# Optimization experiments

Measured on AMD Instinct MI355X. Metric: run time of the kernel, lower is better.

The kernel has to match this reference:

```python
import jax, jax.numpy as jnp
import numpy as np

B, K, D, E, V, T = 128, 49, 512, 256, 10000, 20


def setup_inputs() -> dict:
    key = jax.random.key(0)
    ks = jax.random.split(key, 20)
    rn = lambda k, shape, s=0.02: jax.random.normal(k, shape, jnp.float32) * s
    lengths = jnp.sort(jax.random.randint(ks[3], (B,), 1, T + 1))[::-1]
    lengths = lengths.at[0].set(T)  # max(lengths) == T, sorted descending
    return {
        "spatial": jax.random.normal(ks[0], (B, K, D), jnp.float32),
        "global_feats": jax.random.normal(ks[1], (B, D), jnp.float32),
        "captions": jax.random.randint(ks[2], (B, T), 0, V),
        "lengths": lengths,
        "emb": rn(ks[4], (V, E), 0.05),
        "W_init_h": rn(ks[5], (D, D)), "b_init_h": jnp.zeros((D,), jnp.float32),
        "W_init_m": rn(ks[6], (D, D)), "b_init_m": jnp.zeros((D,), jnp.float32),
        "W_ih": rn(ks[7], (4 * D, E + D)), "b_ih": jnp.zeros((4 * D,), jnp.float32),
        "W_hh": rn(ks[8], (4 * D, D)), "b_hh": jnp.zeros((4 * D,), jnp.float32),
        "Wv": rn(ks[9], (K, D)), "bv": jnp.zeros((K,), jnp.float32),
        "Wg": rn(ks[10], (K, D)), "bg": jnp.zeros((K,), jnp.float32),
        "wh": rn(ks[11], (1, K)), "bh_att": jnp.zeros((1,), jnp.float32),
        "Wp": rn(ks[12], (V, D)), "bp": jnp.zeros((V,), jnp.float32),
    }


def reference(spatial, global_feats, captions, lengths, emb,
              W_init_h, b_init_h, W_init_m, b_init_m,
              W_ih, b_ih, W_hh, b_hh,
              Wv, bv, Wg, bg, wh, bh_att, Wp, bp):
    # initialize_state
    h0 = global_feats @ W_init_h.T + b_init_h  # [B,D]
    m0 = global_feats @ W_init_m.T + b_init_m
    emb_seq = emb[captions]                     # [B,T,E]
    V_proj = spatial @ Wv.T + bv                # [B,K,K] (attn hidden = k), loop-invariant

    def step(carry, xs):
        h, m = carry
        w, t = xs                               # w: [B,E]
        active = (lengths > t)[:, None]         # masked equivalent of shrinking batch
        x = jnp.concatenate([w, global_feats], axis=1)  # [B,E+D]
        gates = x @ W_ih.T + b_ih + h @ W_hh.T + b_hh   # [B,4D]
        i, f, g, o = jnp.split(gates, 4, axis=1)        # torch LSTMCell gate order
        i, f, o = jax.nn.sigmoid(i), jax.nn.sigmoid(f), jax.nn.sigmoid(o)
        g = jnp.tanh(g)
        m_new = f * m + i * g
        h_new = o * jnp.tanh(m_new)
        h = jnp.where(active, h_new, h)
        m = jnp.where(active, m_new, m)
        # spatial attention: z = w_h^T tanh(W_v V + W_g h)
        z = jnp.tanh(V_proj + (h @ Wg.T + bg)[:, None, :]) @ wh[0] + bh_att[0]  # [B,K]
        alpha = jax.nn.softmax(z, axis=1)
        c = jnp.einsum('bk,bkd->bd', alpha, spatial)
        logit = (c + h) @ Wp.T + bp             # [B,V]
        logit = jnp.where(active, logit, 0.0)
        return (h, m), logit

    xs = (emb_seq.transpose(1, 0, 2), jnp.arange(T))
    (_, _), logits = jax.lax.scan(step, (h0, m0), xs)
    return logits.transpose(1, 0, 2)            # [B,T,V]
```

## Files before the change

kernel.cpp:

```cpp
#include <hip/hip_runtime.h>
#include <hip/hip_bf16.h>
#include <math.h>

typedef __bf16 bf16;
typedef __bf16 v8bf __attribute__((ext_vector_type(8)));
typedef __bf16 v4bfv __attribute__((ext_vector_type(4)));
typedef float  v4f  __attribute__((ext_vector_type(4)));

#define B_   128
#define KK_  49
#define D_   512
#define E_   256
#define V_   10000
#define T_   20
#define NG_  2048
#define XK_  768
#define VPAD 10112
#define NP_  128
#define NBLK 64
#define LGRID 256

#define FLG_CNT    1024
#define FLG_READY  1040
#define FLG_LEADER 1056
#define FLG_DONE   1057

#define GLOAD_LDS16(gp, lp) \
    __builtin_amdgcn_global_load_lds((const __attribute__((address_space(1))) void*)(gp), \
                                     (__attribute__((address_space(3))) void*)(lp), 16, 0, 0)

__device__ inline v4bfv cvt4(float4 v) {
    v4bfv o; o[0] = (bf16)v.x; o[1] = (bf16)v.y; o[2] = (bf16)v.z; o[3] = (bf16)v.w;
    return o;
}

__device__ inline float fsig(float x) {
    return __fdividef(1.f, 1.f + __expf(-x));
}
__device__ inline float ftanh(float x) {
    return 1.f - 2.f * __fdividef(1.f, 1.f + __expf(2.f * x));
}

__global__ void prep_kernel(
    const float* __restrict__ spatial, const float* __restrict__ gfeat,
    const int* __restrict__ caps, const float* __restrict__ emb,
    const float* __restrict__ W_init_h, const float* __restrict__ b_init_h,
    const float* __restrict__ W_init_m, const float* __restrict__ b_init_m,
    const float* __restrict__ W_ih, const float* __restrict__ b_ih,
    const float* __restrict__ W_hh, const float* __restrict__ b_hh,
    const float* __restrict__ Wv, const float* __restrict__ bv,
    const float* __restrict__ Wg, const float* __restrict__ bg,
    const float* __restrict__ Wp,
    bf16* __restrict__ Wp_b, bf16* __restrict__ Whh_b, bf16* __restrict__ Wih_b,
    bf16* __restrict__ Xin_b, bf16* __restrict__ Sp_b,
    bf16* __restrict__ Wv_b, bf16* __restrict__ Wg_b,
    bf16* __restrict__ Winit2_b, bf16* __restrict__ Gf_b,
    float* __restrict__ bias_comb, float* __restrict__ bias_init,
    float* __restrict__ bv_pad, float* __restrict__ bg_pad,
    int* __restrict__ flags)
{
    const int stride = gridDim.x * blockDim.x;
    const int tid0 = blockIdx.x * blockDim.x + threadIdx.x;
    const float4 z4 = make_float4(0.f, 0.f, 0.f, 0.f);

    for (int i = tid0; i < NBLK * 32; i += stride) flags[i] = 0;

    for (int i4 = tid0; i4 < VPAD * D_ / 4; i4 += stride) {
        int row = i4 >> 7;
        float4 v = (row < V_) ? ((const float4*)Wp)[i4] : z4;
        ((v4bfv*)Wp_b)[i4] = cvt4(v);
    }
    for (int i4 = tid0; i4 < NG_ * D_ / 4; i4 += stride)
        ((v4bfv*)Whh_b)[i4] = cvt4(((const float4*)W_hh)[i4]);
    for (int i4 = tid0; i4 < NG_ * XK_ / 4; i4 += stride)
        ((v4bfv*)Wih_b)[i4] = cvt4(((const float4*)W_ih)[i4]);
    for (int i4 = tid0; i4 < T_ * B_ * XK_ / 4; i4 += stride) {
        int r = i4 / (XK_ / 4), c4 = i4 - r * (XK_ / 4);
        int c = c4 * 4;
        int t = r >> 7, b = r & 127;
        float4 v;
        if (c < E_) v = *(const float4*)&emb[(long)caps[b * T_ + t] * E_ + c];
        else        v = *(const float4*)&gfeat[(long)b * D_ + (c - E_)];
        ((v4bfv*)Xin_b)[i4] = cvt4(v);
    }
    for (int i4 = tid0; i4 < B_ * KK_ * D_ / 4; i4 += stride)
        ((v4bfv*)Sp_b)[i4] = cvt4(((const float4*)spatial)[i4]);
    for (int i4 = tid0; i4 < NP_ * D_ / 4; i4 += stride) {
        int row = i4 >> 7;
        ((v4bfv*)Wv_b)[i4] = cvt4((row < KK_) ? ((const float4*)Wv)[i4] : z4);
        ((v4bfv*)Wg_b)[i4] = cvt4((row < KK_) ? ((const float4*)Wg)[i4] : z4);
    }
    for (int i4 = tid0; i4 < 2 * D_ * D_ / 4; i4 += stride) {
        int row = i4 >> 7;
        float4 v = (row < D_) ? ((const float4*)W_init_h)[i4]
                              : ((const float4*)W_init_m)[i4 - D_ * (D_ / 4)];
        ((v4bfv*)Winit2_b)[i4] = cvt4(v);
    }
    for (int i4 = tid0; i4 < B_ * D_ / 4; i4 += stride)
        ((v4bfv*)Gf_b)[i4] = cvt4(((const float4*)gfeat)[i4]);
    for (int i = tid0; i < NG_; i += stride) bias_comb[i] = b_ih[i] + b_hh[i];
    for (int i = tid0; i < 2 * D_; i += stride)
        bias_init[i] = (i < D_) ? b_init_h[i] : b_init_m[i - D_];
    for (int i = tid0; i < NP_; i += stride) {
        bv_pad[i] = (i < KK_) ? bv[i] : 0.f;
        bg_pad[i] = (i < KK_) ? bg[i] : 0.f;
    }
}

template <int OUTMODE>
__global__ __launch_bounds__(256, 4) void gemm_bt(
    const bf16* __restrict__ A, const bf16* __restrict__ Bm,
    const float* __restrict__ bias, void* __restrict__ Cout, void* __restrict__ Cout2,
    int M, int N, int K, int out_stride, int n_real, const int* __restrict__ lengths)
{
    __shared__ bf16 As[2 * 128 * 32];
    __shared__ bf16 Bs[2 * 128 * 32];
    const int m0 = blockIdx.x * 128, n0 = blockIdx.y * 128;
    const int tid = threadIdx.x;
    const int w = tid >> 6, l = tid & 63;
    const int wm = (w >> 1) * 64, wn = (w & 1) * 64;
    const int lr = l & 15, lq = l >> 4;

    v4f acc[4][4] = {};

    for (int k0 = 0; k0 < K; k0 += 64) {
        __syncthreads();
        #pragma unroll
        for (int c = 0; c < 4; c++) {
            int u = c * 256 + tid;
            int h = u >> 9, v = u & 511;
            int row = v >> 2, kc = (v & 3) * 8;
            int u0 = c * 256 + (tid & ~63);
            GLOAD_LDS16(&A[(long)(m0 + row) * K + k0 + h * 32 + kc], &As[u0 * 8]);
            GLOAD_LDS16(&Bm[(long)(n0 + row) * K + k0 + h * 32 + kc], &Bs[u0 * 8]);
        }
        __syncthreads();
        #pragma unroll
        for (int h = 0; h < 2; h++) {
            v8bf af[4], bfv[4];
            #pragma unroll
            for (int s = 0; s < 4; s++) {
                af[s]  = *(const v8bf*)&As[h * 4096 + (wm + s * 16 + lr) * 32 + lq * 8];
                bfv[s] = *(const v8bf*)&Bs[h * 4096 + (wn + s * 16 + lr) * 32 + lq * 8];
            }
            #pragma unroll
            for (int i = 0; i < 4; i++)
                #pragma unroll
                for (int j = 0; j < 4; j++)
                    acc[i][j] = __builtin_amdgcn_mfma_f32_16x16x32_bf16(af[i], bfv[j], acc[i][j], 0, 0, 0);
        }
    }

    #pragma unroll
    for (int i = 0; i < 4; i++)
        #pragma unroll
        for (int j = 0; j < 4; j++)
            #pragma unroll
            for (int r = 0; r < 4; r++) {
                int m = m0 + wm + i * 16 + lq * 4 + r;
                int n = n0 + wn + j * 16 + lr;
                float v = acc[i][j][r];
                if (OUTMODE == 2) {
                    if (n < n_real) {
                        int t = m % T_, b = m / T_;
                        float o = (t < lengths[b]) ? (v + bias[n]) : 0.f;
                        ((float*)Cout)[(long)m * out_stride + n] = o;
                    }
                } else if (OUTMODE == 3) {
                    if (n < D_) ((bf16*)Cout)[(long)m * D_ + n] = (bf16)(v + bias[n]);
                    else ((float*)Cout2)[(long)m * D_ + n - D_] = v + bias[n];
                } else {
                    ((float*)Cout)[(long)m * out_stride + n] = v + bias[n];
                }
            }
}

__global__ __launch_bounds__(256) void lstm_persist(
    bf16* __restrict__ Hb16, const bf16* __restrict__ Whh_b,
    const float* __restrict__ Xpre, const float* __restrict__ mbuf,
    const int* __restrict__ lengths, int* __restrict__ flags)
{
    __shared__ bf16 Bl[128][520];
    __shared__ int s_info[2];
    const int tid = threadIdx.x;

    if (tid == 0) {
        int xcd;
        asm volatile("s_getreg_b32 %0, hwreg(HW_REG_XCC_ID)" : "=s"(xcd));
        xcd &= 15;
        int slot = __hip_atomic_fetch_add(&flags[FLG_CNT + xcd], 1,
                                          __ATOMIC_RELAXED, __HIP_MEMORY_SCOPE_AGENT);
        if (slot == 31) {
            int exp = 0;
            bool win = __hip_atomic_compare_exchange_strong(
                &flags[FLG_LEADER], &exp, xcd + 1,
                __ATOMIC_RELAXED, __ATOMIC_RELAXED, __HIP_MEMORY_SCOPE_AGENT);
            __hip_atomic_store(&flags[FLG_READY + xcd], win ? 1 : 2,
                               __ATOMIC_RELAXED, __HIP_MEMORY_SCOPE_AGENT);
        }
        int st;
        if (slot < 32) {
            int dn;
            do {
                st = __hip_atomic_load(&flags[FLG_READY + xcd],
                                       __ATOMIC_RELAXED, __HIP_MEMORY_SCOPE_AGENT);
                dn = __hip_atomic_load(&flags[FLG_DONE],
                                       __ATOMIC_RELAXED, __HIP_MEMORY_SCOPE_AGENT);
            } while (st == 0 && dn == 0);
            if (st == 0) st = 2;
        } else st = 2;
        s_info[0] = st;
        s_info[1] = slot;
    }
    __syncthreads();
    if (s_info[0] != 1) return;

    const int slot = s_info[1];
    const int w = tid >> 6, l = tid & 63;
    const int lr = l & 15, lq = l >> 4;
    const int rh = slot & 1;
    const int d0v = (slot >> 1) * 32;
    const int b0 = rh * 64;
    int* const prog = &flags[rh ? 64 : 0];

    for (int u = tid; u < 128 * 64; u += 256) {
        int row = u >> 6, kc = (u & 63) * 8;
        int g = row >> 5, dd = row & 31;
        *(v8bf*)&Bl[row][kc] = *(const v8bf*)&Whh_b[(long)(g * D_ + d0v + dd) * D_ + kc];
    }

    const int brow = b0 + w * 16 + lq * 4;
    float m_st[4][2], h_st[4][2], xpf[4][2][4];
    int lenr[4];
    #pragma unroll
    for (int r = 0; r < 4; r++) {
        int b = brow + r;
        lenr[r] = lengths[b];
        #pragma unroll
        for (int dh = 0; dh < 2; dh++) {
            int d = d0v + dh * 16 + lr;
            m_st[r][dh] = mbuf[(long)b * D_ + d];
            h_st[r][dh] = (float)Hb16[(long)b * D_ + d];
            #pragma unroll
            for (int g = 0; g < 4; g++)
                xpf[r][dh][g] = Xpre[(long)b * NG_ + g * D_ + d];
        }
    }
    __syncthreads();

    for (int t = 0; t < T_; t++) {
        const bf16* Arow = Hb16 + (long)t * B_ * D_ + (long)(b0 + w * 16 + lr) * D_;
        v4f acc[8] = {};
        #pragma unroll
        for (int kk = 0; kk < 16; kk++) {
            v8bf a = *(const v8bf*)&Arow[kk * 32 + lq * 8];
            #pragma unroll
            for (int nt = 0; nt < 8; nt++) {
                v8bf bv = *(const v8bf*)&Bl[nt * 16 + lr][kk * 32 + lq * 8];
                acc[nt] = __builtin_amdgcn_mfma_f32_16x16x32_bf16(a, bv, acc[nt], 0, 0, 0);
            }
        }

        bf16* hn = Hb16 + (long)(t + 1) * B_ * D_;
        #pragma unroll
        for (int r = 0; r < 4; r++) {
            int b = brow + r;
            bool active = t < lenr[r];
            #pragma unroll
            for (int dh = 0; dh < 2; dh++) {
                float gi = fsig (acc[0 + dh][r] + xpf[r][dh][0]);
                float gf = fsig (acc[2 + dh][r] + xpf[r][dh][1]);
                float gc = ftanh(acc[4 + dh][r] + xpf[r][dh][2]);
                float go = fsig (acc[6 + dh][r] + xpf[r][dh][3]);
                float m_new = gf * m_st[r][dh] + gi * gc;
                float h_new = go * ftanh(m_new);
                m_st[r][dh] = active ? m_new : m_st[r][dh];
                h_st[r][dh] = active ? h_new : h_st[r][dh];
                hn[(long)b * D_ + d0v + dh * 16 + lr] = (bf16)h_st[r][dh];
            }
        }

        if (t + 1 < T_) {
            __syncthreads();
            if (tid == 0) {
                const int target = 16 * (t + 1);
                int c = __hip_atomic_fetch_add(prog, 1,
                          __ATOMIC_RELAXED, __HIP_MEMORY_SCOPE_AGENT) + 1;
                while (c < target)
                    c = __hip_atomic_fetch_add(prog, 0,
                          __ATOMIC_RELAXED, __HIP_MEMORY_SCOPE_AGENT);
            }
            #pragma unroll
            for (int r = 0; r < 4; r++) {
                int b = brow + r;
                #pragma unroll
                for (int dh = 0; dh < 2; dh++)
                    #pragma unroll
                    for (int g = 0; g < 4; g++)
                        xpf[r][dh][g] = Xpre[(long)(t + 1) * B_ * NG_ + (long)b * NG_
                                             + g * D_ + d0v + dh * 16 + lr];
            }
            __syncthreads();
        }
    }

    if (slot == 0 && tid == 0)
        __hip_atomic_store(&flags[FLG_DONE], 1, __ATOMIC_RELAXED, __HIP_MEMORY_SCOPE_AGENT);
}

__global__ __launch_bounds__(256) void attn_kernel(
    const bf16* __restrict__ Hb16, const float* __restrict__ g_all,
    const float* __restrict__ Vproj, const float* __restrict__ wh,
    const bf16* __restrict__ Sp_b, bf16* __restrict__ ctx)
{
    const int w = threadIdx.x >> 6, l = threadIdx.x & 63;
    const int b = blockIdx.x / 5, tg = blockIdx.x % 5;
    const int t = tg * 4 + w;
    const int r = t * 128 + b;
    __shared__ float svp[KK_][53];
    __shared__ float sg[4][64], sal[4][64], swh[64];

    for (int p = threadIdx.x; p < KK_ * 64; p += 256) {
        int k = p >> 6, j = p & 63;
        if (j < KK_) svp[k][j] = Vproj[((long)b * KK_ + k) * NP_ + j];
    }
    if (w == 0) swh[l] = (l < KK_) ? wh[l] : 0.f;
    sg[w][l] = (l < KK_) ? g_all[(long)r * NP_ + l] : 0.f;
    __syncthreads();

    float z = -1e30f;
    if (l < KK_) {
        float a = 0.f;
        for (int j = 0; j < KK_; j++)
            a += swh[j] * ftanh(svp[l][j] + sg[w][j]);
        z = a;
    }
    float mx = z;
    #pragma unroll
    for (int o = 32; o > 0; o >>= 1) mx = fmaxf(mx, __shfl_xor(mx, o));
    float e = (l < KK_) ? __expf(z - mx) : 0.f;
    float sm = e;
    #pragma unroll
    for (int o = 32; o > 0; o >>= 1) sm += __shfl_xor(sm, o);
    sal[w][l] = e / sm;
    __syncthreads();

    const bf16* hrow = Hb16 + (long)(t + 1) * B_ * D_ + (long)b * D_;
    const bf16* sp = Sp_b + (long)b * KK_ * D_;
    bf16* crow = ctx + (long)(b * T_ + t) * D_;
    v8bf hro = *(const v8bf*)&hrow[l * 8];
    float c[8] = {};
    for (int k = 0; k < KK_; k++) {
        v8bf s8 = *(const v8bf*)&sp[k * D_ + l * 8];
        float al = sal[w][k];
        #pragma unroll
        for (int e2 = 0; e2 < 8; e2++) c[e2] += al * (float)s8[e2];
    }
    v8bf outv;
    #pragma unroll
    for (int e2 = 0; e2 < 8; e2++) outv[e2] = (bf16)(c[e2] + (float)hro[e2]);
    *(v8bf*)&crow[l * 8] = outv;
}

extern "C" void kernel_launch(void* const* d_in, const int* in_sizes, int n_in,
                              void* d_out, int out_size, void* d_ws, size_t ws_size,
                              hipStream_t stream)
{
    const float* spatial  = (const float*)d_in[0];
    const float* gfeat    = (const float*)d_in[1];
    const int*   caps     = (const int*)d_in[2];
    const int*   lengths  = (const int*)d_in[3];
    const float* emb      = (const float*)d_in[4];
    const float* W_init_h = (const float*)d_in[5];
    const float* b_init_h = (const float*)d_in[6];
    const float* W_init_m = (const float*)d_in[7];
    const float* b_init_m = (const float*)d_in[8];
    const float* W_ih     = (const float*)d_in[9];
    const float* b_ih     = (const float*)d_in[10];
    const float* W_hh     = (const float*)d_in[11];
    const float* b_hh     = (const float*)d_in[12];
    const float* Wv       = (const float*)d_in[13];
    const float* bv       = (const float*)d_in[14];
    const float* Wg       = (const float*)d_in[15];
    const float* bg       = (const float*)d_in[16];
    const float* wh       = (const float*)d_in[17];
    const float* bh_att   = (const float*)d_in[18];
    const float* Wp       = (const float*)d_in[19];
    const float* bp       = (const float*)d_in[20];
    float* out = (float*)d_out;
    (void)bh_att;

    char* ws = (char*)d_ws;
    size_t off = 0;
    auto alloc = [&](size_t bytes) -> void* {
        off = (off + 255) & ~(size_t)255;
        void* p = ws + off;
        off += bytes;
        return p;
    };

    bf16* Wp_b    = (bf16*)alloc((size_t)VPAD * D_ * 2);
    bf16* Whh_b   = (bf16*)alloc((size_t)NG_ * D_ * 2);
    bf16* Wih_b   = (bf16*)alloc((size_t)NG_ * XK_ * 2);
    bf16* Xin_b   = (bf16*)alloc((size_t)T_ * B_ * XK_ * 2);
    bf16* Sp_b    = (bf16*)alloc((size_t)B_ * KK_ * D_ * 2);
    bf16* Wv_b    = (bf16*)alloc((size_t)NP_ * D_ * 2);
    bf16* Wg_b    = (bf16*)alloc((size_t)NP_ * D_ * 2);
    bf16* Winit2_b= (bf16*)alloc((size_t)2 * D_ * D_ * 2);
    bf16* Gf_b    = (bf16*)alloc((size_t)B_ * D_ * 2);
    float* bias_comb = (float*)alloc(NG_ * 4);
    float* bias_init = (float*)alloc(2 * D_ * 4);
    float* bv_pad    = (float*)alloc(NP_ * 4);
    float* bg_pad    = (float*)alloc(NP_ * 4);
    bf16* Hb16    = (bf16*)alloc((size_t)(T_ + 1) * B_ * D_ * 2);
    float* mbuf   = (float*)alloc((size_t)B_ * D_ * 4);
    float* Xpre   = (float*)alloc((size_t)T_ * B_ * NG_ * 4);
    float* VprojW = (float*)alloc((size_t)B_ * KK_ * NP_ * 4);
    float* g_allW = (float*)alloc((size_t)T_ * B_ * NP_ * 4);
    bf16* ctx     = (bf16*)alloc((size_t)T_ * B_ * D_ * 2);
    int*  flags   = (int*)alloc((size_t)NBLK * 32 * 4);

    prep_kernel<<<1024, 256, 0, stream>>>(
        spatial, gfeat, caps, emb, W_init_h, b_init_h, W_init_m, b_init_m,
        W_ih, b_ih, W_hh, b_hh, Wv, bv, Wg, bg, Wp,
        Wp_b, Whh_b, Wih_b, Xin_b, Sp_b, Wv_b, Wg_b, Winit2_b, Gf_b,
        bias_comb, bias_init, bv_pad, bg_pad, flags);

    gemm_bt<3><<<dim3(1, 8), 256, 0, stream>>>(Gf_b, Winit2_b, bias_init,
                                               Hb16, mbuf, B_, 2 * D_, D_, 0, 0, nullptr);

    gemm_bt<0><<<dim3((B_ * KK_) / 128, 1), 256, 0, stream>>>(
        Sp_b, Wv_b, bv_pad, VprojW, nullptr, B_ * KK_, NP_, D_, NP_, 0, nullptr);

    gemm_bt<0><<<dim3((T_ * B_) / 128, NG_ / 128), 256, 0, stream>>>(
        Xin_b, Wih_b, bias_comb, Xpre, nullptr, T_ * B_, NG_, XK_, NG_, 0, nullptr);

    lstm_persist<<<LGRID, 256, 0, stream>>>(Hb16, Whh_b, Xpre, mbuf, lengths, flags);

    gemm_bt<0><<<dim3((T_ * B_) / 128, 1), 256, 0, stream>>>(
        Hb16 + (size_t)B_ * D_, Wg_b, bg_pad, g_allW, nullptr, T_ * B_, NP_, D_, NP_, 0, nullptr);

    attn_kernel<<<B_ * 5, 256, 0, stream>>>(Hb16, g_allW, VprojW, wh, Sp_b, ctx);

    gemm_bt<2><<<dim3((T_ * B_) / 128, VPAD / 128), 256, 0, stream>>>(
        ctx, Wp_b, bp, out, nullptr, T_ * B_, VPAD, D_, V_, V_, lengths);
}
```

Measured before the change: 477.7 us.

## Replace block barriers in persistent LSTM with LDS flag handshake and preload A

The two __syncthreads around the cross-block step barrier are replaced with LDS atomic counters. Each wave signals arrival, thread 0 does the global progress handshake, and the waves spin on a release flag. Waves other than wave 0 prefetch the next step's Xpre gate inputs while the global wait is in flight, so that load latency overlaps the barrier. The A-row loads for the MFMA loop are also hoisted into a register array before the compute loop, at the cost of more registers and extra spin-waiting logic. Memory ordering for the global h writes now relies on the relaxed agent atomics without a workgroup barrier, which risks a correctness issue.

Result: no change. 481.0 us (+0.7%).

```diff
diff --git a/kernel.cpp b/kernel.cpp
--- a/kernel.cpp
+++ b/kernel.cpp
@@ -182,9 +182,12 @@
 {
     __shared__ bf16 Bl[128][520];
     __shared__ int s_info[2];
+    __shared__ int s_arr[2];
+    __shared__ int s_rel;
     const int tid = threadIdx.x;
 
     if (tid == 0) {
+        s_arr[0] = 0; s_arr[1] = 0; s_rel = 0;
         int xcd;
         asm volatile("s_getreg_b32 %0, hwreg(HW_REG_XCC_ID)" : "=s"(xcd));
         xcd &= 15;
@@ -250,14 +253,17 @@
 
     for (int t = 0; t < T_; t++) {
         const bf16* Arow = Hb16 + (long)t * B_ * D_ + (long)(b0 + w * 16 + lr) * D_;
+        v8bf a[16];
+        #pragma unroll
+        for (int kk = 0; kk < 16; kk++)
+            a[kk] = *(const v8bf*)&Arow[kk * 32 + lq * 8];
         v4f acc[8] = {};
         #pragma unroll
         for (int kk = 0; kk < 16; kk++) {
-            v8bf a = *(const v8bf*)&Arow[kk * 32 + lq * 8];
             #pragma unroll
             for (int nt = 0; nt < 8; nt++) {
                 v8bf bv = *(const v8bf*)&Bl[nt * 16 + lr][kk * 32 + lq * 8];
-                acc[nt] = __builtin_amdgcn_mfma_f32_16x16x32_bf16(a, bv, acc[nt], 0, 0, 0);
+                acc[nt] = __builtin_amdgcn_mfma_f32_16x16x32_bf16(a[kk], bv, acc[nt], 0, 0, 0);
             }
         }
 
@@ -281,26 +287,50 @@
         }
 
         if (t + 1 < T_) {
-            __syncthreads();
+            const int nxt = t + 1;
+            if (l == 0)
+                __hip_atomic_fetch_add(&s_arr[t & 1], 1,
+                                       __ATOMIC_RELEASE, __HIP_MEMORY_SCOPE_WORKGROUP);
             if (tid == 0) {
-                const int target = 16 * (t + 1);
-                int c = __hip_atomic_fetch_add(prog, 1,
-                          __ATOMIC_RELAXED, __HIP_MEMORY_SCOPE_AGENT) + 1;
-                while (c < target)
-                    c = __hip_atomic_fetch_add(prog, 0,
-                          __ATOMIC_RELAXED, __HIP_MEMORY_SCOPE_AGENT);
-            }
-            #pragma unroll
-            for (int r = 0; r < 4; r++) {
-                int b = brow + r;
+                while (__hip_atomic_load(&s_arr[t & 1],
+                        __ATOMIC_ACQUIRE, __HIP_MEMORY_SCOPE_WORKGROUP) < 4) {}
+                __hip_atomic_store(&s_arr[t & 1], 0,
+                                   __ATOMIC_RELAXED, __HIP_MEMORY_SCOPE_WORKGROUP);
+                __hip_atomic_fetch_add(prog, 1,
+                                       __ATOMIC_RELAXED, __HIP_MEMORY_SCOPE_AGENT);
+                const int target = 16 * nxt;
+                while (__hip_atomic_load(prog,
+                        __ATOMIC_RELAXED, __HIP_MEMORY_SCOPE_AGENT) < target) {}
+                __hip_atomic_store(&s_rel, nxt,
+                                   __ATOMIC_RELEASE, __HIP_MEMORY_SCOPE_WORKGROUP);
+            }
+            if (w != 0) {
                 #pragma unroll
-                for (int dh = 0; dh < 2; dh++)
+                for (int r = 0; r < 4; r++) {
+                    int b = brow + r;
                     #pragma unroll
-                    for (int g = 0; g < 4; g++)
-                        xpf[r][dh][g] = Xpre[(long)(t + 1) * B_ * NG_ + (long)b * NG_
-                                             + g * D_ + d0v + dh * 16 + lr];
-            }
-            __syncthreads();
+                    for (int dh = 0; dh < 2; dh++)
+                        #pragma unroll
+                        for (int g = 0; g < 4; g++)
+                            xpf[r][dh][g] = Xpre[(long)nxt * B_ * NG_ + (long)b * NG_
+                                                 + g * D_ + d0v + dh * 16 + lr];
+                }
+                while (__hip_atomic_load(&s_rel,
+                        __ATOMIC_ACQUIRE, __HIP_MEMORY_SCOPE_WORKGROUP) < nxt) {}
+            } else {
+                while (__hip_atomic_load(&s_rel,
+                        __ATOMIC_ACQUIRE, __HIP_MEMORY_SCOPE_WORKGROUP) < nxt) {}
+                #pragma unroll
+                for (int r = 0; r < 4; r++) {
+                    int b = brow + r;
+                    #pragma unroll
+                    for (int dh = 0; dh < 2; dh++)
+                        #pragma unroll
+                        for (int g = 0; g < 4; g++)
+                            xpf[r][dh][g] = Xpre[(long)nxt * B_ * NG_ + (long)b * NG_
+                                                 + g * D_ + d0v + dh * 16 + lr];
+                }
+            }
         }
     }
 
```
